# Kernel tuning notes

Measured on AMD Instinct MI355X. Metric: run time of the kernel, lower is better.

The kernel has to match this reference:

```python
import jax, jax.numpy as jnp
import numpy as np

B, S, D, H, KVH = 1, 2048, 4096, 32, 8
HD = D // H  # head_dim = 128
ROPE_THETA = 500000.0
NEG_INF = -1e9


def setup_inputs() -> dict:
    key = jax.random.key(0)
    ks = jax.random.split(key, 5)
    x = jax.random.normal(ks[0], (B, S, D), jnp.float32)
    wq = jax.random.normal(ks[1], (D, H * HD), jnp.float32) * 0.02
    wk = jax.random.normal(ks[2], (D, KVH * HD), jnp.float32) * 0.02
    wv = jax.random.normal(ks[3], (D, KVH * HD), jnp.float32) * 0.02
    wo = jax.random.normal(ks[4], (H * HD, D), jnp.float32) * 0.02
    inv = 1.0 / (ROPE_THETA ** (np.arange(0, HD, 2, dtype=np.float32) / HD))
    ang = np.arange(S, dtype=np.float32)[:, None] * inv[None, :]  # [S, HD/2]
    return dict(x=x, wq=wq, wk=wk, wv=wv, wo=wo,
                freqs_cos=jnp.asarray(np.cos(ang)), freqs_sin=jnp.asarray(np.sin(ang)))


def _rope(t, cos, sin):
    # t: [B, S, h, HD]; complex rotation on even/odd interleaved pairs
    tr = t.reshape(*t.shape[:-1], HD // 2, 2)
    t0, t1 = tr[..., 0], tr[..., 1]
    c = cos[None, :, None, :]
    s = sin[None, :, None, :]
    o0 = t0 * c - t1 * s
    o1 = t0 * s + t1 * c
    return jnp.stack([o0, o1], axis=-1).reshape(t.shape)


def reference(x, wq, wk, wv, wo, freqs_cos, freqs_sin):
    # QKV projections (prefill path: seqlen>1, start_pos=0 -> causal flash attn)
    xq = (x @ wq).reshape(B, S, H, HD)
    xk = (x @ wk).reshape(B, S, KVH, HD)
    xv = (x @ wv).reshape(B, S, KVH, HD)
    xq = _rope(xq, freqs_cos, freqs_sin)
    xk = _rope(xk, freqs_cos, freqs_sin)
    # GQA: repeat kv heads to match query heads
    n_rep = H // KVH
    xk = jnp.repeat(xk, n_rep, axis=2)  # [B,S,H,HD]
    xv = jnp.repeat(xv, n_rep, axis=2)
    scale = 1.0 / jnp.sqrt(jnp.asarray(HD, xq.dtype))
    scores = jnp.einsum('bqhd,bkhd->bhqk', xq, xk) * scale
    causal = jnp.tril(jnp.ones((S, S), bool))
    scores = jnp.where(causal[None, None], scores, NEG_INF)
    probs = jax.nn.softmax(scores, axis=-1)
    out = jnp.einsum('bhqk,bkhd->bqhd', probs, xv)  # [B,S,H,HD]
    return out.reshape(B, S, H * HD) @ wo
```

## Files before the change

kernel.cpp:

```cpp
#include <hip/hip_runtime.h>
#include <type_traits>

typedef __attribute__((ext_vector_type(8))) short short8;
typedef __attribute__((ext_vector_type(4))) float float4v;

__device__ inline float bf2f(short s) {
    unsigned u = ((unsigned)(unsigned short)s) << 16;
    float f; __builtin_memcpy(&f, &u, 4); return f;
}
__device__ inline short f2bf(float f) {
    unsigned u; __builtin_memcpy(&u, &f, 4);
    unsigned lsb = (u >> 16) & 1;
    u += 0x7fffu + lsb;
    return (short)(u >> 16);
}

__device__ inline void glds16(const void* g, void* l) {
    __builtin_amdgcn_global_load_lds(
        (const __attribute__((address_space(1))) unsigned int*)g,
        (__attribute__((address_space(3))) unsigned int*)l, 16, 0, 0);
}

__global__ __launch_bounds__(256) void conv_f32_bf16(const float* __restrict__ in,
                                                     short* __restrict__ out, int n8) {
    int idx = blockIdx.x * 256 + threadIdx.x;
    if (idx >= n8) return;
    const float* src = in + (size_t)idx * 8;
    float4v a = *(const float4v*)src;
    float4v b = *(const float4v*)(src + 4);
    short8 o;
#pragma unroll
    for (int j = 0; j < 4; j++) { o[j] = f2bf(a[j]); o[4 + j] = f2bf(b[j]); }
    *(short8*)(out + (size_t)idx * 8) = o;
}

__global__ __launch_bounds__(256) void transpose_conv(const float* __restrict__ in,
                                                      short* __restrict__ out,
                                                      int K, int ldn, int noff) {
    __shared__ float t[64 * 65];
    const int n0 = blockIdx.x * 64, k0 = blockIdx.y * 64;
    const int tid = threadIdx.x;
#pragma unroll
    for (int i = 0; i < 4; i++) {
        int slot = tid + 256 * i;
        int row = slot >> 4, c4 = slot & 15;
        float4v v = *(const float4v*)(in + (size_t)(k0 + row) * ldn + noff + n0 + c4 * 4);
#pragma unroll
        for (int j = 0; j < 4; j++) t[row * 65 + c4 * 4 + j] = v[j];
    }
    __syncthreads();
#pragma unroll
    for (int i = 0; i < 2; i++) {
        int slot = tid + 256 * i;
        int row = slot >> 3, c8 = slot & 7;
        short8 v;
#pragma unroll
        for (int j = 0; j < 8; j++) v[j] = f2bf(t[(c8 * 8 + j) * 65 + row]);
        *(short8*)(out + (size_t)(n0 + row) * K + k0 + c8 * 8) = v;
    }
}

__global__ __launch_bounds__(256) void transpose_k(const short* __restrict__ in,
                                                   short* __restrict__ out,
                                                   int K, int N, int ldin) {
    __attribute__((aligned(16))) __shared__ short t[64 * 72];
    const int n0 = blockIdx.x * 64, k0 = blockIdx.y * 64;
    const int tid = threadIdx.x;
#pragma unroll
    for (int i = 0; i < 2; i++) {
        int slot = tid + 256 * i;
        int row = slot >> 3, c8 = slot & 7;
        *(short8*)&t[row * 72 + c8 * 8] =
            *(const short8*)(in + (size_t)(k0 + row) * ldin + n0 + c8 * 8);
    }
    __syncthreads();
#pragma unroll
    for (int i = 0; i < 2; i++) {
        int slot = tid + 256 * i;
        int row = slot >> 3, c8 = slot & 7;
        short8 v;
#pragma unroll
        for (int j = 0; j < 8; j++) v[j] = t[(c8 * 8 + j) * 72 + row];
        *(short8*)(out + (size_t)(n0 + row) * K + k0 + c8 * 8) = v;
    }
}

template <int MF, int NB, typename CT>
__global__ __launch_bounds__(512) void gemm_bt_p(const short* __restrict__ A,
                                                 const short* __restrict__ Bt,
                                                 CT* __restrict__ C) {
    constexpr int BM = MF * 32;
    constexpr int LDC = NB * 256;
    constexpr int APASS = BM / 64;
    __attribute__((aligned(16))) __shared__ short lds[2][(BM + 256) * 64];
    const int tid = threadIdx.x;
    const int lane = tid & 63, wave = tid >> 6;
    const int quad = lane >> 4, l16 = lane & 15;
    const int wm = wave >> 2, wn = wave & 3;
    const int b = blockIdx.x;
    const int sw = (b & 7) * 32 + (b >> 3);
    const int n0 = (sw % NB) * 256;
    const int m0 = (sw / NB) * BM;
    const int lr = lane >> 3, lc = lane & 7;
    const int swc = lc ^ lr;
    const int K = 4096;

    float4v acc[MF][4];
#pragma unroll
    for (int i = 0; i < MF; i++)
#pragma unroll
        for (int j = 0; j < 4; j++) acc[i][j] = (float4v){0.f, 0.f, 0.f, 0.f};

    auto stage = [&](int t, int buf) {
        const int k0 = t * 64;
        short* Ab = &lds[buf][0];
        short* Bb = &lds[buf][BM * 64];
#pragma unroll
        for (int p = 0; p < APASS; p++) {
            int row = p * 64 + wave * 8;
            glds16(A + (size_t)(m0 + row + lr) * K + k0 + swc * 8, Ab + row * 64);
        }
#pragma unroll
        for (int p = 0; p < 4; p++) {
            int row = p * 64 + wave * 8;
            glds16(Bt + (size_t)(n0 + row + lr) * K + k0 + swc * 8, Bb + row * 64);
        }
    };

    stage(0, 0);
    stage(1, 1);

    for (int t = 0; t < 64; t++) {
        if (t + 1 < 64) {
            if constexpr (APASS == 2) asm volatile("s_waitcnt vmcnt(6)" ::: "memory");
            else                      asm volatile("s_waitcnt vmcnt(5)" ::: "memory");
        } else {
            asm volatile("s_waitcnt vmcnt(0)" ::: "memory");
        }
        __builtin_amdgcn_sched_barrier(0);
        __builtin_amdgcn_s_barrier();
        asm volatile("" ::: "memory");
        const short* As = &lds[t & 1][0];
        const short* Bs = &lds[t & 1][BM * 64];
        short8 af[MF][2], bf[4][2];
#pragma unroll
        for (int mf = 0; mf < MF; mf++)
#pragma unroll
            for (int kc = 0; kc < 2; kc++)
                af[mf][kc] = *(const short8*)&As[(wm * MF * 16 + mf * 16 + l16) * 64 +
                                                 (((kc * 4 + quad) ^ (l16 & 7)) * 8)];
#pragma unroll
        for (int nf = 0; nf < 4; nf++)
#pragma unroll
            for (int kc = 0; kc < 2; kc++)
                bf[nf][kc] = *(const short8*)&Bs[(wn * 64 + nf * 16 + l16) * 64 +
                                                 (((kc * 4 + quad) ^ (l16 & 7)) * 8)];
        __builtin_amdgcn_s_setprio(1);
#pragma unroll
        for (int mf = 0; mf < MF; mf++)
#pragma unroll
            for (int nf = 0; nf < 4; nf++)
#pragma unroll
                for (int kc = 0; kc < 2; kc++)
                    acc[mf][nf] = __builtin_amdgcn_mfma_f32_16x16x32_bf16(
                        af[mf][kc], bf[nf][kc], acc[mf][nf], 0, 0, 0);
        __builtin_amdgcn_s_setprio(0);
        asm volatile("" ::: "memory");
        __builtin_amdgcn_s_barrier();
        asm volatile("" ::: "memory");
        if (t + 2 < 64) stage(t + 2, t & 1);
    }

#pragma unroll
    for (int mf = 0; mf < MF; mf++)
#pragma unroll
        for (int nf = 0; nf < 4; nf++) {
            int col = n0 + wn * 64 + nf * 16 + l16;
#pragma unroll
            for (int r = 0; r < 4; r++) {
                int row = m0 + wm * MF * 16 + mf * 16 + quad * 4 + r;
                if constexpr (std::is_same<CT, float>::value)
                    C[(size_t)row * LDC + col] = acc[mf][nf][r];
                else
                    C[(size_t)row * LDC + col] = f2bf(acc[mf][nf][r]);
            }
        }
}

template <typename AT, typename CT>
__global__ __launch_bounds__(256) void gemm_bt_g(const AT* __restrict__ A,
                                                 const short* __restrict__ Bt,
                                                 CT* __restrict__ C,
                                                 int K, int ldc, int coff) {
    __attribute__((aligned(16))) __shared__ short As[128 * 64];
    __attribute__((aligned(16))) __shared__ short Bs[128 * 64];
    const int tid = threadIdx.x;
    const int lane = tid & 63, wave = tid >> 6;
    const int quad = lane >> 4, l16 = lane & 15;
    const int wr = wave >> 1, wc = wave & 1;
    const int m0 = blockIdx.y * 128, n0 = blockIdx.x * 128;
    const int lrow = lane >> 3, lc8 = lane & 7;

    float4v acc[4][4];
#pragma unroll
    for (int i = 0; i < 4; i++)
#pragma unroll
        for (int j = 0; j < 4; j++) acc[i][j] = (float4v){0.f, 0.f, 0.f, 0.f};

    for (int k0 = 0; k0 < K; k0 += 64) {
#pragma unroll
        for (int r = 0; r < 4; r++) {
            int slab = r * 4 + wave;
            glds16(Bt + (size_t)(n0 + slab * 8 + lrow) * K + k0 + lc8 * 8, &Bs[slab * 512]);
        }
        if constexpr (std::is_same<AT, short>::value) {
#pragma unroll
            for (int r = 0; r < 4; r++) {
                int slab = r * 4 + wave;
                glds16(A + (size_t)(m0 + slab * 8 + lrow) * K + k0 + lc8 * 8, &As[slab * 512]);
            }
        } else {
#pragma unroll
            for (int i = 0; i < 4; i++) {
                int slot = tid + 256 * i;
                int row = slot >> 3, c8 = slot & 7;
                const float* src = A + (size_t)(m0 + row) * K + k0 + c8 * 8;
                float4v a = *(const float4v*)src;
                float4v b = *(const float4v*)(src + 4);
                short8 o;
#pragma unroll
                for (int j = 0; j < 4; j++) { o[j] = f2bf(a[j]); o[4 + j] = f2bf(b[j]); }
                *(short8*)&As[row * 64 + c8 * 8] = o;
            }
        }
        __syncthreads();
#pragma unroll
        for (int kc = 0; kc < 2; kc++) {
            short8 afr[4], bfr[4];
#pragma unroll
            for (int rt = 0; rt < 4; rt++)
                afr[rt] = *(const short8*)&As[(wr * 64 + rt * 16 + l16) * 64 + kc * 32 + quad * 8];
#pragma unroll
            for (int ct = 0; ct < 4; ct++)
                bfr[ct] = *(const short8*)&Bs[(wc * 64 + ct * 16 + l16) * 64 + kc * 32 + quad * 8];
#pragma unroll
            for (int rt = 0; rt < 4; rt++)
#pragma unroll
                for (int ct = 0; ct < 4; ct++)
                    acc[rt][ct] = __builtin_amdgcn_mfma_f32_16x16x32_bf16(
                        afr[rt], bfr[ct], acc[rt][ct], 0, 0, 0);
        }
        __syncthreads();
    }
#pragma unroll
    for (int rt = 0; rt < 4; rt++)
#pragma unroll
        for (int ct = 0; ct < 4; ct++) {
            int col = coff + n0 + wc * 64 + ct * 16 + l16;
#pragma unroll
            for (int r = 0; r < 4; r++) {
                int row = m0 + wr * 64 + rt * 16 + quad * 4 + r;
                if constexpr (std::is_same<CT, float>::value)
                    C[(size_t)row * ldc + col] = acc[rt][ct][r];
                else
                    C[(size_t)row * ldc + col] = f2bf(acc[rt][ct][r]);
            }
        }
}

__global__ void rope_kernel(short* __restrict__ T, const float* __restrict__ cosb,
                            const float* __restrict__ sinb, int nheads, int ld) {
    int idx = blockIdx.x * 256 + threadIdx.x;
    int total = 2048 * nheads * 16;
    if (idx >= total) return;
    int chunk = idx & 15;
    int t2 = idx >> 4;
    int hh = t2 % nheads;
    int s = t2 / nheads;
    short* p = T + (size_t)s * ld + hh * 128 + chunk * 8;
    short8 v = *(short8*)p;
    short8 o;
#pragma unroll
    for (int t = 0; t < 4; t++) {
        int i = chunk * 4 + t;
        float c = cosb[s * 64 + i];
        float sn = sinb[s * 64 + i];
        float a = bf2f(v[2 * t]), b = bf2f(v[2 * t + 1]);
        o[2 * t] = f2bf(a * c - b * sn);
        o[2 * t + 1] = f2bf(a * sn + b * c);
    }
    *(short8*)p = o;
}

__global__ __launch_bounds__(256) void attn_kernel(const short* __restrict__ Q,
                                                   const short* __restrict__ K,
                                                   const short* __restrict__ Vt,
                                                   short* __restrict__ O, int ldk) {
    __attribute__((aligned(16))) __shared__ short Ks[2][64 * 128];
    __attribute__((aligned(16))) __shared__ short Vs[2][128 * 64];
    __attribute__((aligned(16))) __shared__ short Ps[4][16 * 72];
    const int tid = threadIdx.x;
    const int lane = tid & 63, wave = tid >> 6;
    const int quad = lane >> 4, l16 = lane & 15;
    const int h = blockIdx.y, kvh = h >> 2;
    const float scale2 = 0.08838834764831845f * 1.4426950408889634f;

    for (int pass = 0; pass < 2; pass++) {
        const int qtile = pass ? (31 - (int)blockIdx.x) : (int)blockIdx.x;
        const int qbase = qtile * 64;
        const int q0 = qbase + wave * 16;
        const int nt = qtile + 1;

        short8 qf[4];
        const short* qrow = Q + (size_t)(q0 + l16) * 4096 + h * 128;
#pragma unroll
        for (int ks = 0; ks < 4; ks++) qf[ks] = *(const short8*)(qrow + ks * 32 + quad * 8);

        float4v o_acc[8];
#pragma unroll
        for (int i = 0; i < 8; i++) o_acc[i] = (float4v){0.f, 0.f, 0.f, 0.f};
        float m_i[4], l_i[4];
#pragma unroll
        for (int r = 0; r < 4; r++) { m_i[r] = -1e9f; l_i[r] = 0.f; }

        short8 kreg[4], vreg[4];
#pragma unroll
        for (int i = 0; i < 4; i++) {
            int slot = tid + 256 * i;
            int row = slot >> 4, c8 = slot & 15;
            kreg[i] = *(const short8*)(K + (size_t)row * ldk + kvh * 128 + c8 * 8);
        }
#pragma unroll
        for (int i = 0; i < 4; i++) {
            int slot = tid + 256 * i;
            int row = slot >> 3, c8 = slot & 7;
            vreg[i] = *(const short8*)(Vt + (size_t)(kvh * 128 + row) * 2048 + c8 * 8);
        }
        __syncthreads();
#pragma unroll
        for (int i = 0; i < 4; i++) {
            int slot = tid + 256 * i;
            int row = slot >> 4, c8 = slot & 15;
            *(short8*)&Ks[0][row * 128 + ((c8 ^ (row & 15)) * 8)] = kreg[i];
        }
#pragma unroll
        for (int i = 0; i < 4; i++) {
            int slot = tid + 256 * i;
            int row = slot >> 3, c8 = slot & 7;
            *(short8*)&Vs[0][row * 64 + ((c8 ^ (row & 7)) * 8)] = vreg[i];
        }

        for (int t = 0; t < nt; t++) {
            const int kv0 = t * 64;
            const int cur = t & 1;
            __syncthreads();
            const bool pf = (t + 1 < nt);
            if (pf) {
                const int kv1 = kv0 + 64;
#pragma unroll
                for (int i = 0; i < 4; i++) {
                    int slot = tid + 256 * i;
                    int row = slot >> 4, c8 = slot & 15;
                    kreg[i] = *(const short8*)(K + (size_t)(kv1 + row) * ldk + kvh * 128 + c8 * 8);
                }
#pragma unroll
                for (int i = 0; i < 4; i++) {
                    int slot = tid + 256 * i;
                    int row = slot >> 3, c8 = slot & 7;
                    vreg[i] = *(const short8*)(Vt + (size_t)(kvh * 128 + row) * 2048 + kv1 + c8 * 8);
                }
            }

            float4v s_acc[4];
#pragma unroll
            for (int i = 0; i < 4; i++) s_acc[i] = (float4v){0.f, 0.f, 0.f, 0.f};
            __builtin_amdgcn_s_setprio(1);
#pragma unroll
            for (int nsub = 0; nsub < 4; nsub++) {
                const int row = nsub * 16 + l16;
#pragma unroll
                for (int ks = 0; ks < 4; ks++) {
                    short8 kf = *(const short8*)&Ks[cur][row * 128 + (((ks * 4 + quad) ^ l16) * 8)];
                    s_acc[nsub] = __builtin_amdgcn_mfma_f32_16x16x32_bf16(
                        qf[ks], kf, s_acc[nsub], 0, 0, 0);
                }
            }
            __builtin_amdgcn_s_setprio(0);

            const bool diag = (t == nt - 1);
            float p[4][4];
#pragma unroll
            for (int nsub = 0; nsub < 4; nsub++)
#pragma unroll
                for (int r = 0; r < 4; r++) {
                    float v = s_acc[nsub][r] * scale2;
                    if (diag) {
                        int rowq = q0 + quad * 4 + r;
                        int col = kv0 + nsub * 16 + l16;
                        v = (col <= rowq) ? v : -1e9f;
                    }
                    p[nsub][r] = v;
                }
            float tm[4];
#pragma unroll
            for (int r = 0; r < 4; r++)
                tm[r] = fmaxf(fmaxf(p[0][r], p[1][r]), fmaxf(p[2][r], p[3][r]));
#pragma unroll
            for (int off = 1; off < 16; off <<= 1)
#pragma unroll
                for (int r = 0; r < 4; r++)
                    tm[r] = fmaxf(tm[r], __shfl_xor(tm[r], off, 64));
            int ok = 1;
#pragma unroll
            for (int r = 0; r < 4; r++) ok &= (tm[r] <= m_i[r]);
            const bool need = !__all(ok);
            float alpha[4];
            if (need) {
#pragma unroll
                for (int r = 0; r < 4; r++) {
                    float mn = fmaxf(m_i[r], tm[r]);
                    alpha[r] = __builtin_amdgcn_exp2f(m_i[r] - mn);
                    m_i[r] = mn;
                }
            }
            float rs[4];
#pragma unroll
            for (int r = 0; r < 4; r++) rs[r] = 0.f;
#pragma unroll
            for (int nsub = 0; nsub < 4; nsub++)
#pragma unroll
                for (int r = 0; r < 4; r++) {
                    float e = __builtin_amdgcn_exp2f(p[nsub][r] - m_i[r]);
                    rs[r] += e;
                    Ps[wave][(quad * 4 + r) * 72 + nsub * 16 + l16] = f2bf(e);
                }
#pragma unroll
            for (int off = 1; off < 16; off <<= 1)
#pragma unroll
                for (int r = 0; r < 4; r++) rs[r] += __shfl_xor(rs[r], off, 64);
            if (need) {
#pragma unroll
                for (int r = 0; r < 4; r++) l_i[r] = l_i[r] * alpha[r] + rs[r];
#pragma unroll
                for (int dt = 0; dt < 8; dt++)
#pragma unroll
                    for (int r = 0; r < 4; r++) o_acc[dt][r] *= alpha[r];
            } else {
#pragma unroll
                for (int r = 0; r < 4; r++) l_i[r] += rs[r];
            }

            short8 pf0 = *(const short8*)&Ps[wave][l16 * 72 + quad * 8];
            short8 pf1 = *(const short8*)&Ps[wave][l16 * 72 + 32 + quad * 8];
            __builtin_amdgcn_s_setprio(1);
#pragma unroll
            for (int dt = 0; dt < 8; dt++) {
                const int row = dt * 16 + l16;
                short8 vf0 = *(const short8*)&Vs[cur][row * 64 + ((quad ^ (l16 & 7)) * 8)];
                short8 vf1 = *(const short8*)&Vs[cur][row * 64 + (((4 + quad) ^ (l16 & 7)) * 8)];
                o_acc[dt] = __builtin_amdgcn_mfma_f32_16x16x32_bf16(pf0, vf0, o_acc[dt], 0, 0, 0);
                o_acc[dt] = __builtin_amdgcn_mfma_f32_16x16x32_bf16(pf1, vf1, o_acc[dt], 0, 0, 0);
            }
            __builtin_amdgcn_s_setprio(0);

            if (pf) {
#pragma unroll
                for (int i = 0; i < 4; i++) {
                    int slot = tid + 256 * i;
                    int row = slot >> 4, c8 = slot & 15;
                    *(short8*)&Ks[cur ^ 1][row * 128 + ((c8 ^ (row & 15)) * 8)] = kreg[i];
                }
#pragma unroll
                for (int i = 0; i < 4; i++) {
                    int slot = tid + 256 * i;
                    int row = slot >> 3, c8 = slot & 7;
                    *(short8*)&Vs[cur ^ 1][row * 64 + ((c8 ^ (row & 7)) * 8)] = vreg[i];
                }
            }
        }

#pragma unroll
        for (int dt = 0; dt < 8; dt++)
#pragma unroll
            for (int r = 0; r < 4; r++) {
                int rowq = q0 + quad * 4 + r;
                O[(size_t)rowq * 4096 + h * 128 + dt * 16 + l16] = f2bf(o_acc[dt][r] / l_i[r]);
            }
    }
}

extern "C" void kernel_launch(void* const* d_in, const int* in_sizes, int n_in,
                              void* d_out, int out_size, void* d_ws, size_t ws_size,
                              hipStream_t stream) {
    (void)in_sizes; (void)n_in; (void)out_size;
    const float* x  = (const float*)d_in[0];
    const float* wq = (const float*)d_in[1];
    const float* wk = (const float*)d_in[2];
    const float* wv = (const float*)d_in[3];
    const float* wo = (const float*)d_in[4];
    const float* fc = (const float*)d_in[5];
    const float* fs = (const float*)d_in[6];
    float* out = (float*)d_out;
    char* ws = (char*)d_ws;
    const size_t MB = 1ull << 20;

    if (ws_size >= 76 * MB) {
        short* xb  = (short*)(ws);
        short* Qb  = (short*)(ws + 16 * MB);
        short* KVb = (short*)(ws + 32 * MB);
        short* Vt  = (short*)(ws + 40 * MB);
        short* WT  = (short*)(ws + 44 * MB);
        conv_f32_bf16<<<4096, 256, 0, stream>>>(x, xb, 2048 * 4096 / 8);
        transpose_conv<<<dim3(64, 64), 256, 0, stream>>>(wq, WT, 4096, 4096, 0);
        gemm_bt_p<4, 16, short><<<256, 512, 0, stream>>>(xb, WT, Qb);
        transpose_conv<<<dim3(16, 64), 256, 0, stream>>>(wk, WT, 4096, 1024, 0);
        transpose_conv<<<dim3(16, 64), 256, 0, stream>>>(wv, WT + (size_t)1024 * 4096, 4096, 1024, 0);
        gemm_bt_p<2, 8, short><<<256, 512, 0, stream>>>(xb, WT, KVb);
        rope_kernel<<<4096, 256, 0, stream>>>(Qb, fc, fs, 32, 4096);
        rope_kernel<<<1024, 256, 0, stream>>>(KVb, fc, fs, 8, 2048);
        transpose_k<<<dim3(16, 32), 256, 0, stream>>>(KVb + 1024, Vt, 2048, 1024, 2048);
        attn_kernel<<<dim3(16, 32), 256, 0, stream>>>(Qb, KVb, Vt, Qb, 2048);
        transpose_conv<<<dim3(64, 64), 256, 0, stream>>>(wo, WT, 4096, 4096, 0);
        gemm_bt_p<4, 16, float><<<256, 512, 0, stream>>>(Qb, WT, out);
    } else if (ws_size >= 60 * MB) {
        short* xb  = (short*)(ws);
        short* Qb  = (short*)(ws + 16 * MB);
        short* KVb = (short*)(ws + 32 * MB);
        short* Vt  = (short*)(ws + 40 * MB);
        short* WT  = (short*)(ws + 44 * MB);
        conv_f32_bf16<<<4096, 256, 0, stream>>>(x, xb, 2048 * 4096 / 8);
        for (int s = 0; s < 2; s++) {
            transpose_conv<<<dim3(32, 64), 256, 0, stream>>>(wq, WT, 4096, 4096, s * 2048);
            gemm_bt_g<short, short><<<dim3(16, 16), 256, 0, stream>>>(xb, WT, Qb, 4096, 4096, s * 2048);
        }
        transpose_conv<<<dim3(16, 64), 256, 0, stream>>>(wk, WT, 4096, 1024, 0);
        transpose_conv<<<dim3(16, 64), 256, 0, stream>>>(wv, WT + (size_t)1024 * 4096, 4096, 1024, 0);
        gemm_bt_g<short, short><<<dim3(16, 16), 256, 0, stream>>>(xb, WT, KVb, 4096, 2048, 0);
        rope_kernel<<<4096, 256, 0, stream>>>(Qb, fc, fs, 32, 4096);
        rope_kernel<<<1024, 256, 0, stream>>>(KVb, fc, fs, 8, 2048);
        transpose_k<<<dim3(16, 32), 256, 0, stream>>>(KVb + 1024, Vt, 2048, 1024, 2048);
        attn_kernel<<<dim3(16, 32), 256, 0, stream>>>(Qb, KVb, Vt, Qb, 2048);
        for (int s = 0; s < 2; s++) {
            transpose_conv<<<dim3(32, 64), 256, 0, stream>>>(wo, WT, 4096, 4096, s * 2048);
            gemm_bt_g<short, float><<<dim3(16, 16), 256, 0, stream>>>(Qb, WT, out, 4096, 4096, s * 2048);
        }
    } else {
        short* WT = (short*)(ws);
        short* Qb = (short*)(ws + 8 * MB);
        short* Kb = (short*)(ws + 24 * MB);
        short* Vb = (short*)(ws + 28 * MB);
        short* Vt = (short*)(ws + 32 * MB);
        for (int s = 0; s < 4; s++) {
            transpose_conv<<<dim3(16, 64), 256, 0, stream>>>(wq, WT, 4096, 4096, s * 1024);
            gemm_bt_g<float, short><<<dim3(8, 16), 256, 0, stream>>>(x, WT, Qb, 4096, 4096, s * 1024);
        }
        transpose_conv<<<dim3(16, 64), 256, 0, stream>>>(wk, WT, 4096, 1024, 0);
        gemm_bt_g<float, short><<<dim3(8, 16), 256, 0, stream>>>(x, WT, Kb, 4096, 1024, 0);
        transpose_conv<<<dim3(16, 64), 256, 0, stream>>>(wv, WT, 4096, 1024, 0);
        gemm_bt_g<float, short><<<dim3(8, 16), 256, 0, stream>>>(x, WT, Vb, 4096, 1024, 0);
        rope_kernel<<<4096, 256, 0, stream>>>(Qb, fc, fs, 32, 4096);
        rope_kernel<<<1024, 256, 0, stream>>>(Kb, fc, fs, 8, 1024);
        transpose_k<<<dim3(16, 32), 256, 0, stream>>>(Vb, Vt, 2048, 1024, 1024);
        attn_kernel<<<dim3(16, 32), 256, 0, stream>>>(Qb, Kb, Vt, Qb, 1024);
        for (int s = 0; s < 4; s++) {
            transpose_conv<<<dim3(16, 64), 256, 0, stream>>>(wo, WT, 4096, 4096, s * 1024);
            gemm_bt_g<short, float><<<dim3(8, 16), 256, 0, stream>>>(Qb, WT, out, 4096, 4096, s * 1024);
        }
    }
}
```

Before: 567.4 us.

## Replace double-buffered K/V shared tiles with single buffer and extra barrier

Shrinks the attention kernel's K and V shared-memory tiles from two buffers to one. Each iteration now writes the register-held tile into LDS between two barriers, then issues the global prefetch of the next tile before compute. This halves the K/V LDS footprint, which may allow more resident blocks per CU. The cost is an extra block-wide synchronization per tile and LDS stores on the critical path before the matmuls.

```diff
diff --git a/kernel.cpp b/kernel.cpp
--- a/kernel.cpp
+++ b/kernel.cpp
@@ -296,8 +296,8 @@
                                                    const short* __restrict__ K,
                                                    const short* __restrict__ Vt,
                                                    short* __restrict__ O, int ldk) {
-    __attribute__((aligned(16))) __shared__ short Ks[2][64 * 128];
-    __attribute__((aligned(16))) __shared__ short Vs[2][128 * 64];
+    __attribute__((aligned(16))) __shared__ short Ks[64 * 128];
+    __attribute__((aligned(16))) __shared__ short Vs[128 * 64];
     __attribute__((aligned(16))) __shared__ short Ps[4][16 * 72];
     const int tid = threadIdx.x;
     const int lane = tid & 63, wave = tid >> 6;
@@ -336,26 +336,24 @@
             int row = slot >> 3, c8 = slot & 7;
             vreg[i] = *(const short8*)(Vt + (size_t)(kvh * 128 + row) * 2048 + c8 * 8);
         }
-        __syncthreads();
-#pragma unroll
-        for (int i = 0; i < 4; i++) {
-            int slot = tid + 256 * i;
-            int row = slot >> 4, c8 = slot & 15;
-            *(short8*)&Ks[0][row * 128 + ((c8 ^ (row & 15)) * 8)] = kreg[i];
-        }
-#pragma unroll
-        for (int i = 0; i < 4; i++) {
-            int slot = tid + 256 * i;
-            int row = slot >> 3, c8 = slot & 7;
-            *(short8*)&Vs[0][row * 64 + ((c8 ^ (row & 7)) * 8)] = vreg[i];
-        }
 
         for (int t = 0; t < nt; t++) {
             const int kv0 = t * 64;
-            const int cur = t & 1;
             __syncthreads();
-            const bool pf = (t + 1 < nt);
-            if (pf) {
+#pragma unroll
+            for (int i = 0; i < 4; i++) {
+                int slot = tid + 256 * i;
+                int row = slot >> 4, c8 = slot & 15;
+                *(short8*)&Ks[row * 128 + ((c8 ^ (row & 15)) * 8)] = kreg[i];
+            }
+#pragma unroll
+            for (int i = 0; i < 4; i++) {
+                int slot = tid + 256 * i;
+                int row = slot >> 3, c8 = slot & 7;
+                *(short8*)&Vs[row * 64 + ((c8 ^ (row & 7)) * 8)] = vreg[i];
+            }
+            __syncthreads();
+            if (t + 1 < nt) {
                 const int kv1 = kv0 + 64;
 #pragma unroll
                 for (int i = 0; i < 4; i++) {
@@ -380,7 +378,7 @@
                 const int row = nsub * 16 + l16;
 #pragma unroll
                 for (int ks = 0; ks < 4; ks++) {
-                    short8 kf = *(const short8*)&Ks[cur][row * 128 + (((ks * 4 + quad) ^ l16) * 8)];
+                    short8 kf = *(const short8*)&Ks[row * 128 + (((ks * 4 + quad) ^ l16) * 8)];
                     s_acc[nsub] = __builtin_amdgcn_mfma_f32_16x16x32_bf16(
                         qf[ks], kf, s_acc[nsub], 0, 0, 0);
                 }
@@ -456,27 +454,12 @@
 #pragma unroll
             for (int dt = 0; dt < 8; dt++) {
                 const int row = dt * 16 + l16;
-                short8 vf0 = *(const short8*)&Vs[cur][row * 64 + ((quad ^ (l16 & 7)) * 8)];
-                short8 vf1 = *(const short8*)&Vs[cur][row * 64 + (((4 + quad) ^ (l16 & 7)) * 8)];
+                short8 vf0 = *(const short8*)&Vs[row * 64 + ((quad ^ (l16 & 7)) * 8)];
+                short8 vf1 = *(const short8*)&Vs[row * 64 + (((4 + quad) ^ (l16 & 7)) * 8)];
                 o_acc[dt] = __builtin_amdgcn_mfma_f32_16x16x32_bf16(pf0, vf0, o_acc[dt], 0, 0, 0);
                 o_acc[dt] = __builtin_amdgcn_mfma_f32_16x16x32_bf16(pf1, vf1, o_acc[dt], 0, 0, 0);
             }
             __builtin_amdgcn_s_setprio(0);
-
-            if (pf) {
-#pragma unroll
-                for (int i = 0; i < 4; i++) {
-                    int slot = tid + 256 * i;
-                    int row = slot >> 4, c8 = slot & 15;
-                    *(short8*)&Ks[cur ^ 1][row * 128 + ((c8 ^ (row & 15)) * 8)] = kreg[i];
-                }
-#pragma unroll
-                for (int i = 0; i < 4; i++) {
-                    int slot = tid + 256 * i;
-                    int row = slot >> 3, c8 = slot & 7;
-                    *(short8*)&Vs[cur ^ 1][row * 64 + ((c8 ^ (row & 7)) * 8)] = vreg[i];
-                }
-            }
         }
 
 #pragma unroll
```

Result: no change. 563.7 us (-0.7%).
